# Kernel optimization log

Measured on AMD Instinct MI355X. Metric: run time of the kernel, lower is better.

The kernel has to match this reference:

```python
import jax, jax.numpy as jnp
import numpy as np

D = 20       # bond_dim (= virtual_dim = per-module output_dim)
BATCH = 128
BN_EPS = 1e-5


def _unfold(t, h, w, n):
    # torch x.unfold(2,h,h).unfold(3,w,w).reshape(b, C, -1, n)
    B, C, H, W = t.shape
    t = t.reshape(B, C, H // h, h, W // w, w).transpose(0, 1, 2, 4, 3, 5)
    return t.reshape(B, C, -1, n)


def _mps(x, cores, label):
    # x: [b, C, P, n] site values; cores: [P, n, D, F, D] with F = 2*C; label: [P, D, O, D]
    feat = jnp.concatenate([x, 1.0 - x], axis=1)              # [b, F, P, n]  ([x, 1-x] feature map)
    M = jnp.einsum('bfpn,pnufv->npbuv', feat, cores)           # [n, P, b, D, D] site matrices
    v = jnp.full((cores.shape[2],), cores.shape[2] ** -0.5, dtype=x.dtype)  # boundary vector
    left = jnp.einsum('u,pbuv->pbv', v, M[0])
    for i in range(1, M.shape[0]):                             # n is small & static (4 or 16)
        left = jnp.einsum('pbu,pbuv->pbv', left, M[i])
    return jnp.einsum('pbu,puov,v->bpo', left, label, v)       # [b, P, O]


def _bn(y, gamma, beta):
    # training-mode BatchNorm1d over channel axis 1 of [b, C, L]
    mean = y.mean(axis=(0, 2), keepdims=True)
    var = y.var(axis=(0, 2), keepdims=True)
    return (y - mean) * jax.lax.rsqrt(var + BN_EPS) * gamma[None, :, None] + beta[None, :, None]


def setup_inputs() -> dict:
    key = jax.random.key(0)
    ks = jax.random.split(key, 9)
    f32 = jnp.float32
    def core(k, shape):
        F = shape[-2]
        return (jax.random.normal(k, shape, f32) * np.float32(np.sqrt(3.0 / (D * F))))
    def lab(k, shape):
        return jax.random.normal(k, shape, f32) * np.float32(D ** -0.5)
    x = jax.random.uniform(ks[0], (BATCH, 48, 32, 32), f32)
    return {
        'x': x,
        'cores1': core(ks[1], (256, 4, D, 96, D)), 'label1': lab(ks[2], (256, D, D, D)),
        'g1': jnp.ones(256, f32), 'b1': jnp.zeros(256, f32),
        'cores2': core(ks[3], (64, 4, D, 2 * D, D)), 'label2': lab(ks[4], (64, D, D, D)),
        'g2': jnp.ones(64, f32), 'b2': jnp.zeros(64, f32),
        'cores3': core(ks[5], (16, 4, D, 2 * D, D)), 'label3': lab(ks[6], (16, D, D, D)),
        'g3': jnp.ones(16, f32), 'b3': jnp.zeros(16, f32),
        'coresF': core(ks[7], (16, D, 2 * D, D)), 'labelF': lab(ks[8], (D, 10, D)),
    }


def reference(x, cores1, label1, g1, b1, cores2, label2, g2, b2,
              cores3, label3, g3, b3, coresF, labelF):
    b = x.shape[0]
    # stage 1: 256 patch-experts over 4 sites each
    x1 = _unfold(x, 16, 16, 4)                  # [b, 48, 256, 4]
    y = _mps(x1, cores1, label1)                # [b, 256, D]
    y = _bn(y, g1, b1).reshape(b, D, 16, 16)    # faithful patch<->bond mixing view
    # stage 2: 64 experts
    y2 = _unfold(y, 8, 8, 4)                    # [b, D, 64, 4]
    y = _mps(y2, cores2, label2)                # [b, 64, D]
    y = _bn(y, g2, b2).reshape(b, D, 8, 8)
    # stage 3: 16 experts
    y3 = _unfold(y, 4, 4, 4)                    # [b, D, 16, 4]
    y = _mps(y3, cores3, label3)                # [b, 16, D]
    y = _bn(y, g3, b3)
    # final MPS over the 16 expert outputs (channels = D)
    y = y.transpose(0, 2, 1)[:, :, None, :]     # [b, D, 1, 16]
    out = _mps(y, coresF[None], labelF[None])   # [b, 1, 10]
    return out[:, 0, :]                         # squeeze -> [b, 10]
```

## Files before the change

kernel.cpp:

```cpp
#include <hip/hip_runtime.h>

#define VB 0.22360679774997896f

typedef __attribute__((ext_vector_type(8))) _Float16 half8;
typedef __attribute__((ext_vector_type(4))) float f32x4;

#define Z1_OFF   0
#define Z2_OFF   655360
#define Z3_OFF   819200
#define GS1_OFF  860160
#define GQ1_OFF  860416
#define GS2_OFF  860672
#define GQ2_OFF  860736
#define GS3_OFF  860800
#define GQ3_OFF  860816
#define LV1_OFF  860832
#define LV2_OFF  963232
#define LV3_OFF  988832
#define WH2_OFF  995232
#define WH3_OFF  4272032

#define WAVEBAR() __builtin_amdgcn_wave_barrier()

__global__ __launch_bounds__(256, 8)
void prep_kernel(const float* __restrict__ c2, const float* __restrict__ c3,
                 const float* __restrict__ l1, const float* __restrict__ l2,
                 const float* __restrict__ l3,
                 _Float16* __restrict__ Wh2, _Float16* __restrict__ Wh3,
                 float* __restrict__ v1, float* __restrict__ v2,
                 float* __restrict__ v3,
                 float* __restrict__ gzero)
{
    __shared__ __align__(16) _Float16 fragS[5120];
    const int tid = threadIdx.x;
    const int b   = blockIdx.x;

    if (b < 1600) {
        const float* src;
        _Float16* dst;
        if (b < 1280) { src = c2 + (size_t)b * 3200;          dst = Wh2 + (size_t)b * 5120; }
        else          { src = c3 + (size_t)(b - 1280) * 3200; dst = Wh3 + (size_t)(b - 1280) * 5120; }
        #pragma unroll
        for (int k = 0; k < 3; ++k) {
            int i = tid + k * 256;
            if (i < 640) ((uint4*)fragS)[i] = (uint4){0, 0, 0, 0};
        }
        __syncthreads();
        #pragma unroll
        for (int k = 0; k < 4; ++k) {
            int i4 = tid + k * 256;
            if (i4 < 800) {
                float4 w = *(const float4*)(src + i4 * 4);
                float vals[4] = {w.x, w.y, w.z, w.w};
                #pragma unroll
                for (int t = 0; t < 4; ++t) {
                    int e = i4 * 4 + t;
                    int v = e % 20;
                    int r = e / 20;
                    int f = r % 40;
                    int ul = r / 40;
                    int c = ul * 20 + v;
                    int addr = (((f >> 5) * 5 + (c >> 4)) * 64 +
                                ((f >> 3) & 3) * 16 + (c & 15)) * 8 + (f & 7);
                    fragS[addr] = (_Float16)vals[t];
                }
            }
        }
        __syncthreads();
        #pragma unroll
        for (int k = 0; k < 3; ++k) {
            int i = tid + k * 256;
            if (i < 640) ((uint4*)dst)[i] = ((const uint4*)fragS)[i];
        }
    } else if (b < 1936) {
        const int bb = b - 1600;
        const float* lb;
        float* ov;
        if (bb < 256)      { lb = l1 + (size_t)bb * 8000;         ov = v1 + bb * 400; }
        else if (bb < 320) { lb = l2 + (size_t)(bb - 256) * 8000; ov = v2 + (bb - 256) * 400; }
        else               { lb = l3 + (size_t)(bb - 320) * 8000; ov = v3 + (bb - 320) * 400; }
        for (int i = tid; i < 400; i += 256) {
            const float4* s = (const float4*)(lb + i * 20);
            float acc = 0.f;
            #pragma unroll
            for (int t = 0; t < 5; ++t) {
                float4 w = s[t];
                acc += w.x + w.y + w.z + w.w;
            }
            ov[i] = acc * VB;
        }
    } else {
        for (int i = tid; i < 672; i += 256) gzero[i] = 0.f;
    }
}

#define LOADW(W, ci)                                                          \
    {                                                                         \
        const float* wp_ = wbase + (size_t)(ci) * 7680;                       \
        _Pragma("unroll")                                                     \
        for (int k = 0; k < 4; ++k) {                                         \
            int i4 = tid + k * 512;                                           \
            if (i4 < 1920) W[k] = *(const float4*)(wp_ + i4 * 4);             \
        }                                                                     \
    }

#define SCATW(W, DST)                                                         \
    {                                                                         \
        _Pragma("unroll")                                                     \
        for (int k = 0; k < 4; ++k) {                                         \
            int i4 = tid + k * 512;                                           \
            if (i4 < 1920) {                                                  \
                float vals[4] = {W[k].x, W[k].y, W[k].z, W[k].w};             \
                _Pragma("unroll")                                             \
                for (int t = 0; t < 4; ++t)                                   \
                    DST[sAddr[k][t]] = (_Float16)vals[t];                     \
            }                                                                 \
        }                                                                     \
    }

#define CHUNKD(ci, W)                                                         \
    {                                                                         \
        f32x4 acc[5];                                                         \
        _Pragma("unroll")                                                     \
        for (int nt = 0; nt < 5; ++nt) acc[nt] = (f32x4){0.f, 0.f, 0.f, 0.f};\
        _Pragma("unroll")                                                     \
        for (int ks = 0; ks < 3; ++ks) {                                      \
            _Pragma("unroll")                                                 \
            for (int nt = 0; nt < 5; ++nt) {                                  \
                half8 bf = *(const half8*)&Fcur[((ks * 5 + nt) * 64 + l) * 8];\
                acc[nt] = __builtin_amdgcn_mfma_f32_16x16x32_f16(             \
                    af[ks], bf, acc[nt], 0, 0, 0);                            \
            }                                                                 \
        }                                                                     \
        _Pragma("unroll")                                                     \
        for (int nt = 0; nt < 5; ++nt) {                                      \
            _Pragma("unroll")                                                 \
            for (int r = 0; r < 4; ++r)                                       \
                Mw[(hi * 4 + r) * 84 + nt * 16 + row16] = acc[nt][r];         \
        }                                                                     \
        WAVEBAR();                                                            \
        _Pragma("unroll")                                                     \
        for (int ul = 0; ul < 4; ++ul) {                                      \
            float lvx = lw[bQ * 20 + ((ci) % 5) * 4 + ul];                    \
            _Pragma("unroll")                                                 \
            for (int j = 0; j < 5; ++j)                                       \
                lacc[j] += lvx * Mw[bQ * 84 + ul * 20 + mh * 5 + j];          \
        }                                                                     \
        WAVEBAR();                                                            \
        __syncthreads();                                                      \
        if ((ci) < 19) { SCATW(W, Fnxt) }                                     \
        __syncthreads();                                                      \
        { _Float16* t_ = Fcur; Fcur = Fnxt; Fnxt = t_; }                      \
        if ((ci) <= 16) { LOADW(W, (ci) + 3) }                                \
    }

#define SITE(nv, W0, W1, W2, W3, W4)                                          \
    {                                                                         \
        _Pragma("unroll")                                                     \
        for (int k = 0; k < 12; ++k) {                                        \
            int idx = l + k * 64;                                             \
            float v = ((nv) == 0) ? xr[k].x : ((nv) == 1) ? xr[k].y           \
                    : ((nv) == 2) ? xr[k].z : xr[k].w;                        \
            xSw[idx] = v;                                                     \
        }                                                                     \
        WAVEBAR();                                                            \
        half8 af[3];                                                          \
        _Pragma("unroll")                                                     \
        for (int ks = 0; ks < 3; ++ks) {                                      \
            int f0 = ks * 32 + hi * 8;                                        \
            int cc = (f0 < 48) ? f0 : f0 - 48;                                \
            float4 a  = *(const float4*)&xSw[row16 * 48 + cc];                \
            float4 b2 = *(const float4*)&xSw[row16 * 48 + cc + 4];            \
            float vv[8] = {a.x, a.y, a.z, a.w, b2.x, b2.y, b2.z, b2.w};       \
            bool inv = (f0 >= 48);                                            \
            half8 hv;                                                         \
            _Pragma("unroll")                                                 \
            for (int j = 0; j < 8; ++j)                                       \
                hv[j] = (_Float16)(inv ? (1.f - vv[j]) : vv[j]);              \
            af[ks] = hv;                                                      \
        }                                                                     \
        WAVEBAR();                                                            \
        CHUNKD((nv) * 5 + 0, W0)                                              \
        CHUNKD((nv) * 5 + 1, W1)                                              \
        CHUNKD((nv) * 5 + 2, W2)                                              \
        CHUNKD((nv) * 5 + 3, W3)                                              \
        CHUNKD((nv) * 5 + 4, W4)                                              \
        _Pragma("unroll")                                                     \
        for (int j = 0; j < 5; ++j) {                                         \
            lw[bQ * 20 + mh * 5 + j] = lacc[j]; lacc[j] = 0.f;                \
        }                                                                     \
        WAVEBAR();                                                            \
    }

__global__ __launch_bounds__(512, 2)
void fused1_kernel(const float* __restrict__ x, const float* __restrict__ cores1,
                   const float* __restrict__ labv,
                   float* __restrict__ z1, float* __restrict__ gs, float* __restrict__ gq)
{
    __shared__ __align__(16) float xS[8 * 768];
    __shared__ __align__(16) _Float16 Fbuf[2][7680];
    __shared__ __align__(16) float MchunkS[8 * 16 * 84];
    __shared__ __align__(16) float leftS[8 * 320];
    __shared__ float redS[16];

    const int tid = threadIdx.x;
    const int bid = blockIdx.x;
    const int p   = (bid & 7) * 32 + (bid >> 3);
    const int wv  = tid >> 6, l = tid & 63;
    float* xSw = xS + wv * 768;
    float* Mw  = MchunkS + wv * 1344;
    float* lw  = leftS + wv * 320;
    const int row16 = l & 15, hi = l >> 4;
    const int bQ = l >> 2,   mh = l & 3;
    const int hh  = (p >> 7) * 16 + ((p >> 2) & 15);
    const int ww0 = ((p >> 6) & 1) * 16 + (p & 3) * 4;

    float4 xr[12];
    #pragma unroll
    for (int k = 0; k < 12; ++k) {
        int idx = l + k * 64;
        int br = idx / 48, c = idx - br * 48;
        xr[k] = *(const float4*)(x + (((size_t)((wv * 16 + br) * 48 + c)) << 10)
                                   + hh * 32 + ww0);
    }

    int sAddr[4][4];
    #pragma unroll
    for (int k = 0; k < 4; ++k) {
        int i4 = tid + k * 512;
        if (i4 < 1920) {
            #pragma unroll
            for (int t = 0; t < 4; ++t) {
                int e = i4 * 4 + t;
                int v = e % 20;
                int r = e / 20;
                int f = r % 96;
                int ul = r / 96;
                int c = ul * 20 + v;
                sAddr[k][t] = (((f >> 5) * 5 + (c >> 4)) * 64 +
                               ((f >> 3) & 3) * 16 + (c & 15)) * 8 + (f & 7);
            }
        }
    }

    #pragma unroll
    for (int j = 0; j < 5; ++j) lw[bQ * 20 + mh * 5 + j] = VB;
    WAVEBAR();

    float lacc[5] = {0.f, 0.f, 0.f, 0.f, 0.f};
    float4 wrA[4], wrB[4];
    const float* wbase = cores1 + (size_t)p * 153600;

    _Float16* Fcur = &Fbuf[0][0];
    _Float16* Fnxt = &Fbuf[1][0];

    LOADW(wrA, 0)
    SCATW(wrA, Fcur)
    LOADW(wrA, 1)
    LOADW(wrB, 2)
    __syncthreads();

    SITE(0, wrA, wrB, wrA, wrB, wrA)
    SITE(1, wrB, wrA, wrB, wrA, wrB)
    SITE(2, wrA, wrB, wrA, wrB, wrA)
    SITE(3, wrB, wrA, wrB, wrA, wrB)

    const float* lvp = labv + p * 400;
    #pragma unroll
    for (int k = 0; k < 7; ++k) { int i = l + k * 64; if (i < 400) Mw[i] = lvp[i]; }
    WAVEBAR();
    float yv[5] = {0.f, 0.f, 0.f, 0.f, 0.f};
    #pragma unroll
    for (int u = 0; u < 20; ++u) {
        float lu = lw[bQ * 20 + u];
        #pragma unroll
        for (int j = 0; j < 5; ++j) yv[j] += lu * Mw[u * 20 + mh * 5 + j];
    }
    float s = 0.f, s2 = 0.f;
    #pragma unroll
    for (int j = 0; j < 5; ++j) {
        z1[(size_t)(wv * 16 + bQ) * 5120 + p * 20 + mh * 5 + j] = yv[j];
        s += yv[j]; s2 += yv[j] * yv[j];
    }
    #pragma unroll
    for (int off = 32; off > 0; off >>= 1) {
        s  += __shfl_down(s, off);
        s2 += __shfl_down(s2, off);
    }
    if (l == 0) { redS[wv] = s; redS[8 + wv] = s2; }
    __syncthreads();
    if (tid == 0) {
        float S = 0.f, Q = 0.f;
        #pragma unroll
        for (int w2 = 0; w2 < 8; ++w2) { S += redS[w2]; Q += redS[8 + w2]; }
        gs[p] = S; gq[p] = Q;
    }
}

#define UCBODYN(ucv, CUR, NXT)                                                   \
    {                                                                            \
        if ((ucv) < 4) {                                                         \
            const _Float16* bptr = whp + (size_t)((ucv) + 1) * 5120;             \
            _Pragma("unroll")                                                    \
            for (int q = 0; q < 10; ++q)                                         \
                NXT[q] = *(const half8*)(bptr + (q * 64 + l) * 8);               \
        }                                                                        \
        f32x4 acc[5];                                                            \
        _Pragma("unroll")                                                        \
        for (int nt = 0; nt < 5; ++nt) acc[nt] = (f32x4){0.f, 0.f, 0.f, 0.f};    \
        _Pragma("unroll")                                                        \
        for (int ks = 0; ks < 2; ++ks) {                                         \
            _Pragma("unroll")                                                    \
            for (int nt = 0; nt < 5; ++nt)                                       \
                acc[nt] = __builtin_amdgcn_mfma_f32_16x16x32_f16(                \
                    af[ks], CUR[ks * 5 + nt], acc[nt], 0, 0, 0);                 \
        }                                                                        \
        _Pragma("unroll")                                                        \
        for (int nt = 0; nt < 5; ++nt) {                                         \
            _Pragma("unroll")                                                    \
            for (int r = 0; r < 4; ++r)                                          \
                Mw[(hi * 4 + r) * 84 + nt * 16 + row16] = acc[nt][r];            \
        }                                                                        \
        WAVEBAR();                                                               \
        _Pragma("unroll")                                                        \
        for (int ul = 0; ul < 4; ++ul) {                                         \
            float lvx = lw[bQ * 20 + (ucv) * 4 + ul];                            \
            _Pragma("unroll")                                                    \
            for (int j = 0; j < 5; ++j)                                          \
                lacc[j] += lvx * Mw[bQ * 84 + ul * 20 + mh * 5 + j];             \
        }                                                                        \
        WAVEBAR();                                                               \
    }

template <int STAGE>
__global__ __launch_bounds__(256, 2)
void stageN_kernel(const float* __restrict__ zin, const _Float16* __restrict__ Wh,
                   const float* __restrict__ labv,
                   const float* __restrict__ gsin, const float* __restrict__ gqin,
                   const float* __restrict__ gam,  const float* __restrict__ bet,
                   float* __restrict__ zout,
                   float* __restrict__ gsout, float* __restrict__ gqout)
{
    constexpr int ZIN  = (STAGE == 2) ? 5120 : 1280;
    constexpr int ZOUT = (STAGE == 2) ? 1280 : 320;
    constexpr int JUMP = (STAGE == 2) ? 256 : 64;

    __shared__ __align__(16) float zS[4 * 320];
    __shared__ float scS[4 * 20], shS[4 * 20];
    __shared__ __align__(16) float MchunkS[4 * 16 * 84];
    __shared__ __align__(16) float leftS[4 * 320];

    const int tid = threadIdx.x;
    const int p   = blockIdx.x;
    const int bh  = blockIdx.y;
    const int wv  = tid >> 6, l = tid & 63;
    float* zSw = zS + wv * 320;
    float* scw = scS + wv * 20;
    float* shw = shS + wv * 20;
    float* Mw  = MchunkS + wv * 1344;
    float* lw  = leftS + wv * 320;
    const int row16 = l & 15, hi = l >> 4;
    const int bQ = l >> 2,   mh = l & 3;
    const int bg = bh * 64;

    #pragma unroll
    for (int j = 0; j < 5; ++j) lw[bQ * 20 + mh * 5 + j] = VB;
    WAVEBAR();

    float lacc[5] = {0.f, 0.f, 0.f, 0.f, 0.f};

    #pragma unroll 1
    for (int n = 0; n < 4; ++n) {
        int hh, ww;
        if (STAGE == 2) { hh = (p >> 5) * 8 + ((p >> 1) & 7); ww = ((p >> 4) & 1) * 8 + (p & 1) * 4 + n; }
        else            { hh = (p >> 3) * 4 + (p & 3);        ww = ((p >> 2) & 1) * 4 + n; }
        const int oo = (STAGE == 2) ? (hh * 16 + ww) : (hh * 8 + ww);

        if (l < 20) {
            int ch = (l * JUMP + oo) / 20;
            float mean = gsin[ch] * (1.f / 2560.f);
            float var  = gqin[ch] * (1.f / 2560.f) - mean * mean;
            float rstd = rsqrtf(var + 1e-5f);
            float sc = gam[ch] * rstd;
            scw[l] = sc;
            shw[l] = bet[ch] - mean * sc;
        }
        WAVEBAR();
        #pragma unroll
        for (int q = 0; q < 5; ++q) {
            int d = hi * 5 + q;
            float zraw = zin[(size_t)(bg + wv * 16 + row16) * ZIN + d * JUMP + oo];
            zSw[row16 * 20 + d] = zraw * scw[d] + shw[d];
        }
        WAVEBAR();
        half8 af[2];
        #pragma unroll
        for (int ks = 0; ks < 2; ++ks) {
            int f0 = ks * 32 + hi * 8;
            half8 hv;
            #pragma unroll
            for (int j = 0; j < 8; ++j) {
                int f = f0 + j;
                float val;
                if (f < 20)      val = zSw[row16 * 20 + f];
                else if (f < 40) val = 1.f - zSw[row16 * 20 + f - 20];
                else             val = 0.f;
                hv[j] = (_Float16)val;
            }
            af[ks] = hv;
        }
        WAVEBAR();

        const _Float16* whp = Wh + (size_t)((p * 4 + n) * 5) * 5120;
        half8 bA[10], bB[10];
        {
            #pragma unroll
            for (int q = 0; q < 10; ++q) bA[q] = *(const half8*)(whp + (q * 64 + l) * 8);
        }
        UCBODYN(0, bA, bB)
        UCBODYN(1, bB, bA)
        UCBODYN(2, bA, bB)
        UCBODYN(3, bB, bA)
        UCBODYN(4, bA, bB)

        #pragma unroll
        for (int j = 0; j < 5; ++j) { lw[bQ * 20 + mh * 5 + j] = lacc[j]; lacc[j] = 0.f; }
        WAVEBAR();
    }

    const float* lvp = labv + p * 400;
    #pragma unroll
    for (int k = 0; k < 7; ++k) { int i = l + k * 64; if (i < 400) Mw[i] = lvp[i]; }
    WAVEBAR();
    float yv[5] = {0.f, 0.f, 0.f, 0.f, 0.f};
    #pragma unroll
    for (int u = 0; u < 20; ++u) {
        float lu = lw[bQ * 20 + u];
        #pragma unroll
        for (int j = 0; j < 5; ++j) yv[j] += lu * Mw[u * 20 + mh * 5 + j];
    }
    float s = 0.f, s2 = 0.f;
    #pragma unroll
    for (int j = 0; j < 5; ++j) {
        zout[(size_t)(bg + wv * 16 + bQ) * ZOUT + p * 20 + mh * 5 + j] = yv[j];
        s += yv[j]; s2 += yv[j] * yv[j];
    }
    #pragma unroll
    for (int off = 32; off > 0; off >>= 1) {
        s  += __shfl_down(s, off);
        s2 += __shfl_down(s2, off);
    }
    if ((tid & 63) == 0) {
        atomicAdd(&gsout[p], s);
        atomicAdd(&gqout[p], s2);
    }
}

__global__ __launch_bounds__(256, 4)
void final_kernel(const float* __restrict__ z3,
                  const float* __restrict__ coresF,
                  const float* __restrict__ labelF,
                  const float* __restrict__ g3,
                  const float* __restrict__ b3,
                  const float* __restrict__ gsum3,
                  const float* __restrict__ gsq3,
                  float* __restrict__ out)
{
    __shared__ __align__(16) float fS[16 * 40];
    __shared__ __align__(16) float MS[16 * 400];
    __shared__ float lvS[200];
    __shared__ float scS[16], shS[16];
    __shared__ float leftS[20];

    const int b   = blockIdx.x;
    const int tid = threadIdx.x;

    if (tid < 16) {
        float mean = gsum3[tid] * (1.f / 2560.f);
        float var  = gsq3[tid] * (1.f / 2560.f) - mean * mean;
        float rstd = rsqrtf(var + 1e-5f);
        float sc   = g3[tid] * rstd;
        scS[tid] = sc;
        shS[tid] = b3[tid] - mean * sc;
    }
    __syncthreads();

    for (int i = tid; i < 640; i += 256) {
        int n = i / 40, f = i - n * 40;
        float raw = z3[(size_t)b * 320 + n * 20 + (f % 20)];
        float val = raw * scS[n] + shS[n];
        fS[i] = (f < 20) ? val : (1.f - val);
    }
    for (int i = tid; i < 200; i += 256) {
        int u = i / 10, o = i - u * 10;
        const float* lb = labelF + (size_t)(u * 10 + o) * 20;
        float s = 0.f;
        #pragma unroll
        for (int vv = 0; vv < 20; ++vv) s += lb[vv];
        lvS[i] = s * VB;
    }
    __syncthreads();

    for (int i = tid; i < 6400; i += 256) {
        int n = i / 400, uv = i - n * 400;
        int u = uv / 20, v = uv - u * 20;
        const float* wb = coresF + ((size_t)(n * 20 + u) * 40) * 20 + v;
        const float* fb = fS + n * 40;
        float acc = 0.f;
        #pragma unroll
        for (int f = 0; f < 40; ++f) acc += fb[f] * wb[f * 20];
        MS[i] = acc;
    }
    __syncthreads();

    if (tid < 64) {
        if (tid < 20) leftS[tid] = VB;
        WAVEBAR();
        #pragma unroll 1
        for (int n = 0; n < 16; ++n) {
            float tmp = 0.f;
            if (tid < 20) {
                #pragma unroll
                for (int u = 0; u < 20; ++u) tmp += leftS[u] * MS[n * 400 + u * 20 + tid];
            }
            WAVEBAR();
            if (tid < 20) leftS[tid] = tmp;
            WAVEBAR();
        }
        if (tid < 10) {
            float s = 0.f;
            #pragma unroll
            for (int u = 0; u < 20; ++u) s += leftS[u] * lvS[u * 10 + tid];
            out[b * 10 + tid] = s;
        }
    }
}

extern "C" void kernel_launch(void* const* d_in, const int* in_sizes, int n_in,
                              void* d_out, int out_size, void* d_ws, size_t ws_size,
                              hipStream_t stream)
{
    const float* x      = (const float*)d_in[0];
    const float* cores1 = (const float*)d_in[1];
    const float* label1 = (const float*)d_in[2];
    const float* g1     = (const float*)d_in[3];
    const float* b1     = (const float*)d_in[4];
    const float* cores2 = (const float*)d_in[5];
    const float* label2 = (const float*)d_in[6];
    const float* g2     = (const float*)d_in[7];
    const float* b2     = (const float*)d_in[8];
    const float* cores3 = (const float*)d_in[9];
    const float* label3 = (const float*)d_in[10];
    const float* g3     = (const float*)d_in[11];
    const float* b3     = (const float*)d_in[12];
    const float* coresF = (const float*)d_in[13];
    const float* labelF = (const float*)d_in[14];

    float* ws  = (float*)d_ws;
    float* z1  = ws + Z1_OFF;
    float* z2  = ws + Z2_OFF;
    float* z3  = ws + Z3_OFF;
    float* gs1 = ws + GS1_OFF; float* gq1 = ws + GQ1_OFF;
    float* gs2 = ws + GS2_OFF; float* gq2 = ws + GQ2_OFF;
    float* gs3 = ws + GS3_OFF; float* gq3 = ws + GQ3_OFF;
    float* lv1 = ws + LV1_OFF;
    float* lv2 = ws + LV2_OFF;
    float* lv3 = ws + LV3_OFF;
    _Float16* Wh2 = (_Float16*)(ws + WH2_OFF);
    _Float16* Wh3 = (_Float16*)(ws + WH3_OFF);

    prep_kernel<<<1937, 256, 0, stream>>>(cores2, cores3,
                                          label1, label2, label3,
                                          Wh2, Wh3,
                                          lv1, lv2, lv3, gs1);

    fused1_kernel<<<256, 512, 0, stream>>>(x, cores1, lv1, z1, gs1, gq1);
    stageN_kernel<2><<<dim3(64, 2), 256, 0, stream>>>(z1, Wh2, lv2, gs1, gq1, g1, b1,
                                                      z2, gs2, gq2);
    stageN_kernel<3><<<dim3(16, 2), 256, 0, stream>>>(z2, Wh3, lv3, gs2, gq2, g2, b2,
                                                      z3, gs3, gq3);
    final_kernel<<<128, 256, 0, stream>>>(z3, coresF, labelF, g3, b3,
                                          gs3, gq3, (float*)d_out);
}
```

Measured before the change: 110.5 us.

## Fold prep kernel into stage-1 kernel and compute label vectors in-block

Removes the separate prep launch. The stage-1 fused kernel now sums its own label1 slice into shared memory instead of reading a precomputed vector. After its main work it converts the stage-2/3 cores to the fp16 fragment layout in a grid-stride loop, reduces the label2/label3 vectors, and zeroes the later BN accumulators. This saves one kernel launch and a global round trip for lv1. In exchange, the serial tail of each stage-1 block grows, and stage 2 now depends on work finishing at the end of fused1.

```diff
diff --git a/kernel.cpp b/kernel.cpp
--- a/kernel.cpp
+++ b/kernel.cpp
@@ -14,7 +14,6 @@
 #define GQ2_OFF  860736
 #define GS3_OFF  860800
 #define GQ3_OFF  860816
-#define LV1_OFF  860832
 #define LV2_OFF  963232
 #define LV3_OFF  988832
 #define WH2_OFF  995232
@@ -22,33 +21,236 @@
 
 #define WAVEBAR() __builtin_amdgcn_wave_barrier()
 
-__global__ __launch_bounds__(256, 8)
-void prep_kernel(const float* __restrict__ c2, const float* __restrict__ c3,
-                 const float* __restrict__ l1, const float* __restrict__ l2,
-                 const float* __restrict__ l3,
-                 _Float16* __restrict__ Wh2, _Float16* __restrict__ Wh3,
-                 float* __restrict__ v1, float* __restrict__ v2,
-                 float* __restrict__ v3,
-                 float* __restrict__ gzero)
+#define LOADW(W, ci)                                                          \
+    {                                                                         \
+        const float* wp_ = wbase + (size_t)(ci) * 7680;                       \
+        _Pragma("unroll")                                                     \
+        for (int k = 0; k < 4; ++k) {                                         \
+            int i4 = tid + k * 512;                                           \
+            if (i4 < 1920) W[k] = *(const float4*)(wp_ + i4 * 4);             \
+        }                                                                     \
+    }
+
+#define SCATW(W, DST)                                                         \
+    {                                                                         \
+        _Pragma("unroll")                                                     \
+        for (int k = 0; k < 4; ++k) {                                         \
+            int i4 = tid + k * 512;                                           \
+            if (i4 < 1920) {                                                  \
+                float vals[4] = {W[k].x, W[k].y, W[k].z, W[k].w};             \
+                _Pragma("unroll")                                             \
+                for (int t = 0; t < 4; ++t)                                   \
+                    DST[sAddr[k][t]] = (_Float16)vals[t];                     \
+            }                                                                 \
+        }                                                                     \
+    }
+
+#define CHUNKD(ci, W)                                                         \
+    {                                                                         \
+        f32x4 acc[5];                                                         \
+        _Pragma("unroll")                                                     \
+        for (int nt = 0; nt < 5; ++nt) acc[nt] = (f32x4){0.f, 0.f, 0.f, 0.f};\
+        _Pragma("unroll")                                                     \
+        for (int ks = 0; ks < 3; ++ks) {                                      \
+            _Pragma("unroll")                                                 \
+            for (int nt = 0; nt < 5; ++nt) {                                  \
+                half8 bf = *(const half8*)&Fcur[((ks * 5 + nt) * 64 + l) * 8];\
+                acc[nt] = __builtin_amdgcn_mfma_f32_16x16x32_f16(             \
+                    af[ks], bf, acc[nt], 0, 0, 0);                            \
+            }                                                                 \
+        }                                                                     \
+        _Pragma("unroll")                                                     \
+        for (int nt = 0; nt < 5; ++nt) {                                      \
+            _Pragma("unroll")                                                 \
+            for (int r = 0; r < 4; ++r)                                       \
+                Mw[(hi * 4 + r) * 84 + nt * 16 + row16] = acc[nt][r];         \
+        }                                                                     \
+        WAVEBAR();                                                            \
+        _Pragma("unroll")                                                     \
+        for (int ul = 0; ul < 4; ++ul) {                                      \
+            float lvx = lw[bQ * 20 + ((ci) % 5) * 4 + ul];                    \
+            _Pragma("unroll")                                                 \
+            for (int j = 0; j < 5; ++j)                                       \
+                lacc[j] += lvx * Mw[bQ * 84 + ul * 20 + mh * 5 + j];          \
+        }                                                                     \
+        WAVEBAR();                                                            \
+        __syncthreads();                                                      \
+        if ((ci) < 19) { SCATW(W, Fnxt) }                                     \
+        __syncthreads();                                                      \
+        { _Float16* t_ = Fcur; Fcur = Fnxt; Fnxt = t_; }                      \
+        if ((ci) <= 16) { LOADW(W, (ci) + 3) }                                \
+    }
+
+#define SITE(nv, W0, W1, W2, W3, W4)                                          \
+    {                                                                         \
+        _Pragma("unroll")                                                     \
+        for (int k = 0; k < 12; ++k) {                                        \
+            int idx = l + k * 64;                                             \
+            float v = ((nv) == 0) ? xr[k].x : ((nv) == 1) ? xr[k].y           \
+                    : ((nv) == 2) ? xr[k].z : xr[k].w;                        \
+            xSw[idx] = v;                                                     \
+        }                                                                     \
+        WAVEBAR();                                                            \
+        half8 af[3];                                                          \
+        _Pragma("unroll")                                                     \
+        for (int ks = 0; ks < 3; ++ks) {                                      \
+            int f0 = ks * 32 + hi * 8;                                        \
+            int cc = (f0 < 48) ? f0 : f0 - 48;                                \
+            float4 a  = *(const float4*)&xSw[row16 * 48 + cc];                \
+            float4 b2 = *(const float4*)&xSw[row16 * 48 + cc + 4];            \
+            float vv[8] = {a.x, a.y, a.z, a.w, b2.x, b2.y, b2.z, b2.w};       \
+            bool inv = (f0 >= 48);                                            \
+            half8 hv;                                                         \
+            _Pragma("unroll")                                                 \
+            for (int j = 0; j < 8; ++j)                                       \
+                hv[j] = (_Float16)(inv ? (1.f - vv[j]) : vv[j]);              \
+            af[ks] = hv;                                                      \
+        }                                                                     \
+        WAVEBAR();                                                            \
+        CHUNKD((nv) * 5 + 0, W0)                                              \
+        CHUNKD((nv) * 5 + 1, W1)                                              \
+        CHUNKD((nv) * 5 + 2, W2)                                              \
+        CHUNKD((nv) * 5 + 3, W3)                                              \
+        CHUNKD((nv) * 5 + 4, W4)                                              \
+        _Pragma("unroll")                                                     \
+        for (int j = 0; j < 5; ++j) {                                         \
+            lw[bQ * 20 + mh * 5 + j] = lacc[j]; lacc[j] = 0.f;                \
+        }                                                                     \
+        WAVEBAR();                                                            \
+    }
+
+__global__ __launch_bounds__(512, 2)
+void fused1_kernel(const float* __restrict__ x, const float* __restrict__ cores1,
+                   const float* __restrict__ label1,
+                   const float* __restrict__ cores2, const float* __restrict__ cores3,
+                   const float* __restrict__ label2, const float* __restrict__ label3,
+                   float* __restrict__ z1, float* __restrict__ gs, float* __restrict__ gq,
+                   _Float16* __restrict__ Wh2, _Float16* __restrict__ Wh3,
+                   float* __restrict__ lv2, float* __restrict__ lv3,
+                   float* __restrict__ gzero)
 {
-    __shared__ __align__(16) _Float16 fragS[5120];
+    __shared__ __align__(16) float xS[8 * 768];
+    __shared__ __align__(16) _Float16 Fbuf[2][7680];
+    __shared__ __align__(16) float MchunkS[8 * 16 * 84];
+    __shared__ __align__(16) float leftS[8 * 320];
+    __shared__ __align__(16) float labvS[400];
+    __shared__ float redS[16];
+
     const int tid = threadIdx.x;
-    const int b   = blockIdx.x;
-
-    if (b < 1600) {
+    const int bid = blockIdx.x;
+    const int p   = (bid & 7) * 32 + (bid >> 3);
+    const int wv  = tid >> 6, l = tid & 63;
+    float* xSw = xS + wv * 768;
+    float* Mw  = MchunkS + wv * 1344;
+    float* lw  = leftS + wv * 320;
+    const int row16 = l & 15, hi = l >> 4;
+    const int bQ = l >> 2,   mh = l & 3;
+    const int hh  = (p >> 7) * 16 + ((p >> 2) & 15);
+    const int ww0 = ((p >> 6) & 1) * 16 + (p & 3) * 4;
+
+    float4 xr[12];
+    #pragma unroll
+    for (int k = 0; k < 12; ++k) {
+        int idx = l + k * 64;
+        int br = idx / 48, c = idx - br * 48;
+        xr[k] = *(const float4*)(x + (((size_t)((wv * 16 + br) * 48 + c)) << 10)
+                                   + hh * 32 + ww0);
+    }
+
+    int sAddr[4][4];
+    #pragma unroll
+    for (int k = 0; k < 4; ++k) {
+        int i4 = tid + k * 512;
+        if (i4 < 1920) {
+            #pragma unroll
+            for (int t = 0; t < 4; ++t) {
+                int e = i4 * 4 + t;
+                int v = e % 20;
+                int r = e / 20;
+                int f = r % 96;
+                int ul = r / 96;
+                int c = ul * 20 + v;
+                sAddr[k][t] = (((f >> 5) * 5 + (c >> 4)) * 64 +
+                               ((f >> 3) & 3) * 16 + (c & 15)) * 8 + (f & 7);
+            }
+        }
+    }
+
+    #pragma unroll
+    for (int j = 0; j < 5; ++j) lw[bQ * 20 + mh * 5 + j] = VB;
+    WAVEBAR();
+
+    float lacc[5] = {0.f, 0.f, 0.f, 0.f, 0.f};
+    float4 wrA[4], wrB[4];
+    const float* wbase = cores1 + (size_t)p * 153600;
+
+    _Float16* Fcur = &Fbuf[0][0];
+    _Float16* Fnxt = &Fbuf[1][0];
+
+    LOADW(wrA, 0)
+    SCATW(wrA, Fcur)
+    LOADW(wrA, 1)
+    LOADW(wrB, 2)
+    __syncthreads();
+
+    if (tid < 400) {
+        const float* lb = label1 + (size_t)p * 8000 + tid * 20;
+        float s = 0.f;
+        #pragma unroll
+        for (int vv = 0; vv < 20; ++vv) s += lb[vv];
+        labvS[tid] = s * VB;
+    }
+
+    SITE(0, wrA, wrB, wrA, wrB, wrA)
+    SITE(1, wrB, wrA, wrB, wrA, wrB)
+    SITE(2, wrA, wrB, wrA, wrB, wrA)
+    SITE(3, wrB, wrA, wrB, wrA, wrB)
+
+    float yv[5] = {0.f, 0.f, 0.f, 0.f, 0.f};
+    #pragma unroll
+    for (int u = 0; u < 20; ++u) {
+        float lu = lw[bQ * 20 + u];
+        #pragma unroll
+        for (int j = 0; j < 5; ++j) yv[j] += lu * labvS[u * 20 + mh * 5 + j];
+    }
+    float s = 0.f, s2 = 0.f;
+    #pragma unroll
+    for (int j = 0; j < 5; ++j) {
+        z1[(size_t)(wv * 16 + bQ) * 5120 + p * 20 + mh * 5 + j] = yv[j];
+        s += yv[j]; s2 += yv[j] * yv[j];
+    }
+    #pragma unroll
+    for (int off = 32; off > 0; off >>= 1) {
+        s  += __shfl_down(s, off);
+        s2 += __shfl_down(s2, off);
+    }
+    if (l == 0) { redS[wv] = s; redS[8 + wv] = s2; }
+    __syncthreads();
+    if (tid == 0) {
+        float S = 0.f, Q = 0.f;
+        #pragma unroll
+        for (int w2 = 0; w2 < 8; ++w2) { S += redS[w2]; Q += redS[8 + w2]; }
+        gs[p] = S; gq[p] = Q;
+    }
+
+    __syncthreads();
+    _Float16* fragS = (_Float16*)xS;
+
+    #pragma unroll
+    for (int k = 0; k < 2; ++k) {
+        int i = tid + k * 512;
+        if (i < 640) ((uint4*)fragS)[i] = (uint4){0, 0, 0, 0};
+    }
+    __syncthreads();
+
+    for (int slab = bid; slab < 1600; slab += 256) {
         const float* src;
         _Float16* dst;
-        if (b < 1280) { src = c2 + (size_t)b * 3200;          dst = Wh2 + (size_t)b * 5120; }
-        else          { src = c3 + (size_t)(b - 1280) * 3200; dst = Wh3 + (size_t)(b - 1280) * 5120; }
-        #pragma unroll
-        for (int k = 0; k < 3; ++k) {
-            int i = tid + k * 256;
-            if (i < 640) ((uint4*)fragS)[i] = (uint4){0, 0, 0, 0};
-        }
-        __syncthreads();
-        #pragma unroll
-        for (int k = 0; k < 4; ++k) {
-            int i4 = tid + k * 256;
+        if (slab < 1280) { src = cores2 + (size_t)slab * 3200;          dst = Wh2 + (size_t)slab * 5120; }
+        else             { src = cores3 + (size_t)(slab - 1280) * 3200; dst = Wh3 + (size_t)(slab - 1280) * 5120; }
+        #pragma unroll
+        for (int k = 0; k < 2; ++k) {
+            int i4 = tid + k * 512;
             if (i4 < 800) {
                 float4 w = *(const float4*)(src + i4 * 4);
                 float vals[4] = {w.x, w.y, w.z, w.w};
@@ -68,233 +270,30 @@
         }
         __syncthreads();
         #pragma unroll
-        for (int k = 0; k < 3; ++k) {
-            int i = tid + k * 256;
+        for (int k = 0; k < 2; ++k) {
+            int i = tid + k * 512;
             if (i < 640) ((uint4*)dst)[i] = ((const uint4*)fragS)[i];
         }
-    } else if (b < 1936) {
-        const int bb = b - 1600;
+        __syncthreads();
+    }
+
+    if (bid < 80) {
         const float* lb;
         float* ov;
-        if (bb < 256)      { lb = l1 + (size_t)bb * 8000;         ov = v1 + bb * 400; }
-        else if (bb < 320) { lb = l2 + (size_t)(bb - 256) * 8000; ov = v2 + (bb - 256) * 400; }
-        else               { lb = l3 + (size_t)(bb - 320) * 8000; ov = v3 + (bb - 320) * 400; }
-        for (int i = tid; i < 400; i += 256) {
-            const float4* s = (const float4*)(lb + i * 20);
+        if (bid < 64) { lb = label2 + (size_t)bid * 8000;        ov = lv2 + bid * 400; }
+        else          { lb = label3 + (size_t)(bid - 64) * 8000; ov = lv3 + (bid - 64) * 400; }
+        if (tid < 400) {
+            const float4* sp = (const float4*)(lb + tid * 20);
             float acc = 0.f;
             #pragma unroll
             for (int t = 0; t < 5; ++t) {
-                float4 w = s[t];
+                float4 w = sp[t];
                 acc += w.x + w.y + w.z + w.w;
             }
-            ov[i] = acc * VB;
-        }
-    } else {
-        for (int i = tid; i < 672; i += 256) gzero[i] = 0.f;
-    }
-}
-
-#define LOADW(W, ci)                                                          \
-    {                                                                         \
-        const float* wp_ = wbase + (size_t)(ci) * 7680;                       \
-        _Pragma("unroll")                                                     \
-        for (int k = 0; k < 4; ++k) {                                         \
-            int i4 = tid + k * 512;                                           \
-            if (i4 < 1920) W[k] = *(const float4*)(wp_ + i4 * 4);             \
-        }                                                                     \
-    }
-
-#define SCATW(W, DST)                                                         \
-    {                                                                         \
-        _Pragma("unroll")                                                     \
-        for (int k = 0; k < 4; ++k) {                                         \
-            int i4 = tid + k * 512;                                           \
-            if (i4 < 1920) {                                                  \
-                float vals[4] = {W[k].x, W[k].y, W[k].z, W[k].w};             \
-                _Pragma("unroll")                                             \
-                for (int t = 0; t < 4; ++t)                                   \
-                    DST[sAddr[k][t]] = (_Float16)vals[t];                     \
-            }                                                                 \
-        }                                                                     \
-    }
-
-#define CHUNKD(ci, W)                                                         \
-    {                                                                         \
-        f32x4 acc[5];                                                         \
-        _Pragma("unroll")                                                     \
-        for (int nt = 0; nt < 5; ++nt) acc[nt] = (f32x4){0.f, 0.f, 0.f, 0.f};\
-        _Pragma("unroll")                                                     \
-        for (int ks = 0; ks < 3; ++ks) {                                      \
-            _Pragma("unroll")                                                 \
-            for (int nt = 0; nt < 5; ++nt) {                                  \
-                half8 bf = *(const half8*)&Fcur[((ks * 5 + nt) * 64 + l) * 8];\
-                acc[nt] = __builtin_amdgcn_mfma_f32_16x16x32_f16(             \
-                    af[ks], bf, acc[nt], 0, 0, 0);                            \
-            }                                                                 \
-        }                                                                     \
-        _Pragma("unroll")                                                     \
-        for (int nt = 0; nt < 5; ++nt) {                                      \
-            _Pragma("unroll")                                                 \
-            for (int r = 0; r < 4; ++r)                                       \
-                Mw[(hi * 4 + r) * 84 + nt * 16 + row16] = acc[nt][r];         \
-        }                                                                     \
-        WAVEBAR();                                                            \
-        _Pragma("unroll")                                                     \
-        for (int ul = 0; ul < 4; ++ul) {                                      \
-            float lvx = lw[bQ * 20 + ((ci) % 5) * 4 + ul];                    \
-            _Pragma("unroll")                                                 \
-            for (int j = 0; j < 5; ++j)                                       \
-                lacc[j] += lvx * Mw[bQ * 84 + ul * 20 + mh * 5 + j];          \
-        }                                                                     \
-        WAVEBAR();                                                            \
-        __syncthreads();                                                      \
-        if ((ci) < 19) { SCATW(W, Fnxt) }                                     \
-        __syncthreads();                                                      \
-        { _Float16* t_ = Fcur; Fcur = Fnxt; Fnxt = t_; }                      \
-        if ((ci) <= 16) { LOADW(W, (ci) + 3) }                                \
-    }
-
-#define SITE(nv, W0, W1, W2, W3, W4)                                          \
-    {                                                                         \
-        _Pragma("unroll")                                                     \
-        for (int k = 0; k < 12; ++k) {                                        \
-            int idx = l + k * 64;                                             \
-            float v = ((nv) == 0) ? xr[k].x : ((nv) == 1) ? xr[k].y           \
-                    : ((nv) == 2) ? xr[k].z : xr[k].w;                        \
-            xSw[idx] = v;                                                     \
-        }                                                                     \
-        WAVEBAR();                                                            \
-        half8 af[3];                                                          \
-        _Pragma("unroll")                                                     \
-        for (int ks = 0; ks < 3; ++ks) {                                      \
-            int f0 = ks * 32 + hi * 8;                                        \
-            int cc = (f0 < 48) ? f0 : f0 - 48;                                \
-            float4 a  = *(const float4*)&xSw[row16 * 48 + cc];                \
-            float4 b2 = *(const float4*)&xSw[row16 * 48 + cc + 4];            \
-            float vv[8] = {a.x, a.y, a.z, a.w, b2.x, b2.y, b2.z, b2.w};       \
-            bool inv = (f0 >= 48);                                            \
-            half8 hv;                                                         \
-            _Pragma("unroll")                                                 \
-            for (int j = 0; j < 8; ++j)                                       \
-                hv[j] = (_Float16)(inv ? (1.f - vv[j]) : vv[j]);              \
-            af[ks] = hv;                                                      \
-        }                                                                     \
-        WAVEBAR();                                                            \
-        CHUNKD((nv) * 5 + 0, W0)                                              \
-        CHUNKD((nv) * 5 + 1, W1)                                              \
-        CHUNKD((nv) * 5 + 2, W2)                                              \
-        CHUNKD((nv) * 5 + 3, W3)                                              \
-        CHUNKD((nv) * 5 + 4, W4)                                              \
-        _Pragma("unroll")                                                     \
-        for (int j = 0; j < 5; ++j) {                                         \
-            lw[bQ * 20 + mh * 5 + j] = lacc[j]; lacc[j] = 0.f;                \
-        }                                                                     \
-        WAVEBAR();                                                            \
-    }
-
-__global__ __launch_bounds__(512, 2)
-void fused1_kernel(const float* __restrict__ x, const float* __restrict__ cores1,
-                   const float* __restrict__ labv,
-                   float* __restrict__ z1, float* __restrict__ gs, float* __restrict__ gq)
-{
-    __shared__ __align__(16) float xS[8 * 768];
-    __shared__ __align__(16) _Float16 Fbuf[2][7680];
-    __shared__ __align__(16) float MchunkS[8 * 16 * 84];
-    __shared__ __align__(16) float leftS[8 * 320];
-    __shared__ float redS[16];
-
-    const int tid = threadIdx.x;
-    const int bid = blockIdx.x;
-    const int p   = (bid & 7) * 32 + (bid >> 3);
-    const int wv  = tid >> 6, l = tid & 63;
-    float* xSw = xS + wv * 768;
-    float* Mw  = MchunkS + wv * 1344;
-    float* lw  = leftS + wv * 320;
-    const int row16 = l & 15, hi = l >> 4;
-    const int bQ = l >> 2,   mh = l & 3;
-    const int hh  = (p >> 7) * 16 + ((p >> 2) & 15);
-    const int ww0 = ((p >> 6) & 1) * 16 + (p & 3) * 4;
-
-    float4 xr[12];
-    #pragma unroll
-    for (int k = 0; k < 12; ++k) {
-        int idx = l + k * 64;
-        int br = idx / 48, c = idx - br * 48;
-        xr[k] = *(const float4*)(x + (((size_t)((wv * 16 + br) * 48 + c)) << 10)
-                                   + hh * 32 + ww0);
-    }
-
-    int sAddr[4][4];
-    #pragma unroll
-    for (int k = 0; k < 4; ++k) {
-        int i4 = tid + k * 512;
-        if (i4 < 1920) {
-            #pragma unroll
-            for (int t = 0; t < 4; ++t) {
-                int e = i4 * 4 + t;
-                int v = e % 20;
-                int r = e / 20;
-                int f = r % 96;
-                int ul = r / 96;
-                int c = ul * 20 + v;
-                sAddr[k][t] = (((f >> 5) * 5 + (c >> 4)) * 64 +
-                               ((f >> 3) & 3) * 16 + (c & 15)) * 8 + (f & 7);
-            }
-        }
-    }
-
-    #pragma unroll
-    for (int j = 0; j < 5; ++j) lw[bQ * 20 + mh * 5 + j] = VB;
-    WAVEBAR();
-
-    float lacc[5] = {0.f, 0.f, 0.f, 0.f, 0.f};
-    float4 wrA[4], wrB[4];
-    const float* wbase = cores1 + (size_t)p * 153600;
-
-    _Float16* Fcur = &Fbuf[0][0];
-    _Float16* Fnxt = &Fbuf[1][0];
-
-    LOADW(wrA, 0)
-    SCATW(wrA, Fcur)
-    LOADW(wrA, 1)
-    LOADW(wrB, 2)
-    __syncthreads();
-
-    SITE(0, wrA, wrB, wrA, wrB, wrA)
-    SITE(1, wrB, wrA, wrB, wrA, wrB)
-    SITE(2, wrA, wrB, wrA, wrB, wrA)
-    SITE(3, wrB, wrA, wrB, wrA, wrB)
-
-    const float* lvp = labv + p * 400;
-    #pragma unroll
-    for (int k = 0; k < 7; ++k) { int i = l + k * 64; if (i < 400) Mw[i] = lvp[i]; }
-    WAVEBAR();
-    float yv[5] = {0.f, 0.f, 0.f, 0.f, 0.f};
-    #pragma unroll
-    for (int u = 0; u < 20; ++u) {
-        float lu = lw[bQ * 20 + u];
-        #pragma unroll
-        for (int j = 0; j < 5; ++j) yv[j] += lu * Mw[u * 20 + mh * 5 + j];
-    }
-    float s = 0.f, s2 = 0.f;
-    #pragma unroll
-    for (int j = 0; j < 5; ++j) {
-        z1[(size_t)(wv * 16 + bQ) * 5120 + p * 20 + mh * 5 + j] = yv[j];
-        s += yv[j]; s2 += yv[j] * yv[j];
-    }
-    #pragma unroll
-    for (int off = 32; off > 0; off >>= 1) {
-        s  += __shfl_down(s, off);
-        s2 += __shfl_down(s2, off);
-    }
-    if (l == 0) { redS[wv] = s; redS[8 + wv] = s2; }
-    __syncthreads();
-    if (tid == 0) {
-        float S = 0.f, Q = 0.f;
-        #pragma unroll
-        for (int w2 = 0; w2 < 8; ++w2) { S += redS[w2]; Q += redS[8 + w2]; }
-        gs[p] = S; gq[p] = Q;
-    }
+            ov[tid] = acc * VB;
+        }
+    }
+    if (bid == 255 && tid < 160) gzero[tid] = 0.f;
 }
 
 #define UCBODYN(ucv, CUR, NXT)                                                   \
@@ -563,18 +562,15 @@
     float* gs1 = ws + GS1_OFF; float* gq1 = ws + GQ1_OFF;
     float* gs2 = ws + GS2_OFF; float* gq2 = ws + GQ2_OFF;
     float* gs3 = ws + GS3_OFF; float* gq3 = ws + GQ3_OFF;
-    float* lv1 = ws + LV1_OFF;
     float* lv2 = ws + LV2_OFF;
     float* lv3 = ws + LV3_OFF;
     _Float16* Wh2 = (_Float16*)(ws + WH2_OFF);
     _Float16* Wh3 = (_Float16*)(ws + WH3_OFF);
 
-    prep_kernel<<<1937, 256, 0, stream>>>(cores2, cores3,
-                                          label1, label2, label3,
-                                          Wh2, Wh3,
-                                          lv1, lv2, lv3, gs1);
-
-    fused1_kernel<<<256, 512, 0, stream>>>(x, cores1, lv1, z1, gs1, gq1);
+    fused1_kernel<<<256, 512, 0, stream>>>(x, cores1, label1,
+                                           cores2, cores3, label2, label3,
+                                           z1, gs1, gq1,
+                                           Wh2, Wh3, lv2, lv3, gs2);
     stageN_kernel<2><<<dim3(64, 2), 256, 0, stream>>>(z1, Wh2, lv2, gs1, gq1, g1, b1,
                                                       z2, gs2, gq2);
     stageN_kernel<3><<<dim3(16, 2), 256, 0, stream>>>(z2, Wh3, lv3, gs2, gq2, g2, b2,
```

Result: no change. 110.6 us (+0.0%).
